# Kernel optimization log

Hardware: AMD Instinct MI355X
Metric: run time of the kernel (lower is better)

Reference implementation:

```python
import jax, jax.numpy as jnp
import numpy as np

H = 1024
L = 2

def setup_inputs() -> dict:
    key = jax.random.key(0)
    k1, k2, k3, k4, k5 = jax.random.split(key, 5)
    B, S = 32, 2048
    scale = 1.0 / np.sqrt(H)
    return {
        "query": jax.random.normal(k1, (B, 1, H * L), dtype=jnp.float32),
        "keys": jax.random.normal(k2, (B, S, H), dtype=jnp.float32),
        "Wa_w": jax.random.normal(k3, (H * L, H), dtype=jnp.float32) * scale,
        "Wa_b": jnp.zeros((H,), dtype=jnp.float32),
        "Ua_w": jax.random.normal(k4, (H, H), dtype=jnp.float32) * scale,
        "Ua_b": jnp.zeros((H,), dtype=jnp.float32),
        "Va_w": jax.random.normal(k5, (H, 1), dtype=jnp.float32) * scale,
        "Va_b": jnp.zeros((1,), dtype=jnp.float32),
    }

def reference(query, keys, Wa_w, Wa_b, Ua_w, Ua_b, Va_w, Va_b):
    # query: [B,1,H*L], keys: [B,S,H]
    q = jnp.einsum('bqd,dh->bqh', query, Wa_w) + Wa_b   # [B,1,H]
    k = jnp.einsum('bsd,dh->bsh', keys, Ua_w) + Ua_b    # [B,S,H]
    e = jnp.tanh(q + k)                                  # [B,S,H]
    scores = jnp.einsum('bsh,ho->bso', e, Va_w) + Va_b   # [B,S,1]
    scores = scores[:, :, 0][:, None, :]                 # [B,1,S]
    weights = jax.nn.softmax(scores, axis=-1)            # [B,1,S]
    context = jnp.einsum('bqs,bsh->bqh', weights, keys)  # [B,1,H]
    return (context, weights)
```

## Files before the change

kernel.cpp:

```cpp
#include <hip/hip_runtime.h>
#include <hip/hip_bf16.h>


typedef __attribute__((ext_vector_type(8))) short short8;
typedef __attribute__((ext_vector_type(4))) float floatx4;

typedef const __attribute__((address_space(1))) unsigned int gu32;
typedef __attribute__((address_space(3))) unsigned int lu32;

__device__ __forceinline__ unsigned short f2bf(float f) {
    union { float f; unsigned int u; } c; c.f = f;
    unsigned int u = c.u + 0x7fffu + ((c.u >> 16) & 1u);
    return (unsigned short)(u >> 16);
}

__device__ __forceinline__ unsigned int f2bf2(float lo, float hi) {
#if __has_builtin(__builtin_amdgcn_cvt_pk_bf16_f32)
    auto r = __builtin_amdgcn_cvt_pk_bf16_f32(lo, hi);
    unsigned int u; __builtin_memcpy(&u, &r, 4);
    return u;
#else
    return (unsigned int)f2bf(lo) | ((unsigned int)f2bf(hi) << 16);
#endif
}

__device__ __forceinline__ void gld16(const unsigned short* g, unsigned short* l) {
    __builtin_amdgcn_global_load_lds(
        (gu32*)(uintptr_t)g,
        (lu32*)(unsigned int)(uintptr_t)l,
        16, 0, 0);
}

__global__ __launch_bounds__(256) void qproj_k(
    const float* __restrict__ query, const float* __restrict__ Wa,
    const float* __restrict__ Wab, const float* __restrict__ Uab,
    float* __restrict__ qws)
{
    __shared__ float qs[2048];
    __shared__ float red[16*64];
    const int tid = threadIdx.x;
    const int b = blockIdx.x, hc = blockIdx.y;
    #pragma unroll
    for (int i = 0; i < 8; i++) qs[tid + 256*i] = query[b*2048 + tid + 256*i];
    __syncthreads();
    const int hq = tid & 15;
    const int dg = tid >> 4;
    const float4* wp = reinterpret_cast<const float4*>(Wa + (size_t)(dg*128)*1024 + hc*64 + hq*4);
    const float* qp = qs + dg*128;
    float4 a0; a0.x = a0.y = a0.z = a0.w = 0.f;
    float4 a1; a1.x = a1.y = a1.z = a1.w = 0.f;
    #pragma unroll 4
    for (int d = 0; d < 128; d += 2) {
        float q0 = qp[d], q1 = qp[d+1];
        float4 w0 = wp[(size_t)d*256];
        float4 w1 = wp[(size_t)(d+1)*256];
        a0.x += q0*w0.x; a0.y += q0*w0.y; a0.z += q0*w0.z; a0.w += q0*w0.w;
        a1.x += q1*w1.x; a1.y += q1*w1.y; a1.z += q1*w1.z; a1.w += q1*w1.w;
    }
    a0.x += a1.x; a0.y += a1.y; a0.z += a1.z; a0.w += a1.w;
    *reinterpret_cast<float4*>(red + dg*64 + hq*4) = a0;
    __syncthreads();
    if (tid < 64) {
        float v = 0.f;
        #pragma unroll
        for (int g = 0; g < 16; g++) v += red[g*64 + tid];
        int hh = hc*64 + tid;
        qws[b*1024 + hh] = v + Wab[hh] + Uab[hh];
    }
}

__global__ __launch_bounds__(256) void uat_k(const float* __restrict__ Ua,
                                             unsigned short* __restrict__ uat)
{
    __shared__ unsigned short t[64][65];
    const int x = threadIdx.x & 63, yy = threadIdx.x >> 6;
    const int d0 = blockIdx.x*64, h0 = blockIdx.y*64;
    #pragma unroll
    for (int i = 0; i < 16; i++) {
        int y = yy*16 + i;
        t[y][x] = f2bf(Ua[(size_t)(d0+y)*1024 + h0 + x]);
    }
    __syncthreads();
    #pragma unroll
    for (int i = 0; i < 16; i++) {
        int y = yy*16 + i;
        uat[(size_t)(h0+y)*1024 + d0 + x] = t[x][y];
    }
}

__global__ __launch_bounds__(256) void kb16_k(const float* __restrict__ keys,
                                              unsigned short* __restrict__ kb,
                                              unsigned int nf4)
{
    const unsigned int stride = gridDim.x * 256u;
    unsigned int f = blockIdx.x * 256u + threadIdx.x;
    #pragma unroll 4
    for (int it = 0; it < 4; ++it, f += stride) {
        if (f < nf4) {
            unsigned int elem = f << 2;
            unsigned int rg   = elem >> 10;
            unsigned int rem  = elem & 1023u;
            unsigned int g    = rem >> 5;
            unsigned int c    = (rem >> 3) & 3u;
            unsigned int half = (rem >> 2) & 1u;
            unsigned int p    = ((rg & 2047u) >> 1) & 3u;
            float4 v = reinterpret_cast<const float4*>(keys)[f];
            uint2 w;
            w.x = f2bf2(v.x, v.y);
            w.y = f2bf2(v.z, v.w);
            unsigned int dst = rg*1024u + g*32u + ((c ^ p) << 3) + (half << 2);
            *reinterpret_cast<uint2*>(kb + dst) = w;
        }
    }
}

__global__ __launch_bounds__(256) void score_gemm_fast(
    const unsigned short* __restrict__ kb16,
    const unsigned short* __restrict__ uat,
    const float* __restrict__ qws,
    const float* __restrict__ Va,
    float* __restrict__ score,
    int b0)
{
    __shared__ unsigned short aS[2][128*32];
    __shared__ unsigned short bS[2][256*32];
    const int tid = threadIdx.x;
    const int bz = blockIdx.z;
    const int b = b0 + bz;
    const int s0 = blockIdx.x * 128;
    const int h0 = blockIdx.y * 256;
    const int lane = tid & 63, wave = tid >> 6;
    const int quad = lane >> 4, l15 = lane & 15;
    const int wm = (wave & 1) * 64, wn = (wave >> 1) * 128;

    const int srow = lane >> 2;
    const int schunk = (lane & 3) ^ ((srow >> 1) & 3);
    const unsigned short* ubase = uat + (size_t)h0*1024;
    size_t boff[4];
    #pragma unroll
    for (int u = 0; u < 4; u++) {
        int cg = wave*4 + u;
        boff[u] = (size_t)(cg*16 + srow)*1024 + schunk*8;
    }

    const unsigned short* kA = kb16 + (size_t)(bz*2048 + s0)*1024;
    const size_t aoff0 = (size_t)(tid >> 2)*1024 + (size_t)(tid & 3)*8;
    const size_t aoff1 = (size_t)(64 + (tid >> 2))*1024 + (size_t)(tid & 3)*8;

    floatx4 acc[4][8];
    #pragma unroll
    for (int i = 0; i < 4; i++)
        #pragma unroll
        for (int j = 0; j < 8; j++) acc[i][j] = (floatx4)0.0f;

    gld16(kA + aoff0, aS[0] + wave*512);
    gld16(kA + aoff1, aS[0] + 2048 + wave*512);
    #pragma unroll
    for (int u = 0; u < 4; u++)
        gld16(ubase + boff[u], bS[0] + (wave*4 + u)*512);
    __syncthreads();

    int cur = 0;
    for (int kt = 0; kt < 31; ++kt) {
        const int nxt = cur ^ 1;
        const int k1 = (kt + 1) << 5;

        gld16(kA + aoff0 + k1, aS[nxt] + wave*512);
        gld16(kA + aoff1 + k1, aS[nxt] + 2048 + wave*512);
        #pragma unroll
        for (int u = 0; u < 4; u++)
            gld16(ubase + boff[u] + k1, bS[nxt] + (wave*4 + u)*512);

        short8 af[4], bf8[8];
        #pragma unroll
        for (int i = 0; i < 4; i++) {
            int row = wm + 16*i + l15;
            af[i] = *reinterpret_cast<const short8*>(aS[cur] + row*32 + ((quad ^ ((row>>1)&3)) * 8));
        }
        #pragma unroll
        for (int j = 0; j < 8; j++) {
            int row = wn + 16*j + l15;
            bf8[j] = *reinterpret_cast<const short8*>(bS[cur] + row*32 + ((quad ^ ((row>>1)&3)) * 8));
        }
        #pragma unroll
        for (int i = 0; i < 4; i++)
            #pragma unroll
            for (int j = 0; j < 8; j++)
                acc[i][j] = __builtin_amdgcn_mfma_f32_16x16x32_bf16(af[i], bf8[j], acc[i][j], 0, 0, 0);

        __syncthreads();
        cur = nxt;
    }

    {
        short8 af[4], bf8[8];
        #pragma unroll
        for (int i = 0; i < 4; i++) {
            int row = wm + 16*i + l15;
            af[i] = *reinterpret_cast<const short8*>(aS[cur] + row*32 + ((quad ^ ((row>>1)&3)) * 8));
        }
        #pragma unroll
        for (int j = 0; j < 8; j++) {
            int row = wn + 16*j + l15;
            bf8[j] = *reinterpret_cast<const short8*>(bS[cur] + row*32 + ((quad ^ ((row>>1)&3)) * 8));
        }
        #pragma unroll
        for (int i = 0; i < 4; i++)
            #pragma unroll
            for (int j = 0; j < 8; j++)
                acc[i][j] = __builtin_amdgcn_mfma_f32_16x16x32_bf16(af[i], bf8[j], acc[i][j], 0, 0, 0);
    }

    float qv[8], vav[8];
    #pragma unroll
    for (int j = 0; j < 8; j++) {
        int n = h0 + wn + 16*j + l15;
        qv[j]  = qws[b*1024 + n];
        vav[j] = Va[n];
    }
    #pragma unroll
    for (int i = 0; i < 4; i++) {
        #pragma unroll
        for (int r = 0; r < 4; r++) {
            float p = 0.f;
            #pragma unroll
            for (int j = 0; j < 8; j++) {
                float x = qv[j] + acc[i][j][r];
                float e = __expf(2.f * x);
                float t = 1.f - 2.f * __builtin_amdgcn_rcpf(e + 1.f);
                p += vav[j] * t;
            }
            #pragma unroll
            for (int off = 1; off < 16; off <<= 1) p += __shfl_xor(p, off, 64);
            if (l15 == 0) {
                int m = wm + 16*i + quad*4 + r;
                atomicAdd(score + (size_t)b*2048 + s0 + m, p);
            }
        }
    }
}

__global__ __launch_bounds__(256) void softmax_k(const float* __restrict__ score,
                                                 float* __restrict__ out_w)
{
    const int tid = threadIdx.x;
    const int b = blockIdx.x;
    __shared__ float wred[4], wred2[4];
    float sc[8];
    float mx = -3.0e38f;
    #pragma unroll
    for (int i = 0; i < 8; i++) {
        sc[i] = score[(size_t)b*2048 + tid + 256*i];
        mx = fmaxf(mx, sc[i]);
    }
    #pragma unroll
    for (int off = 32; off >= 1; off >>= 1) mx = fmaxf(mx, __shfl_xor(mx, off, 64));
    if ((tid & 63) == 0) wred[tid >> 6] = mx;
    __syncthreads();
    mx = fmaxf(fmaxf(wred[0], wred[1]), fmaxf(wred[2], wred[3]));
    float e[8]; float lsum = 0.f;
    #pragma unroll
    for (int i = 0; i < 8; i++) { e[i] = __expf(sc[i] - mx); lsum += e[i]; }
    #pragma unroll
    for (int off = 32; off >= 1; off >>= 1) lsum += __shfl_xor(lsum, off, 64);
    if ((tid & 63) == 0) wred2[tid >> 6] = lsum;
    __syncthreads();
    float inv = 1.0f / (wred2[0] + wred2[1] + wred2[2] + wred2[3]);
    #pragma unroll
    for (int i = 0; i < 8; i++) out_w[b*2048 + tid + 256*i] = e[i] * inv;
}

__global__ __launch_bounds__(256) void ctx_k(const float* __restrict__ keys,
                                             const float* __restrict__ w,
                                             float* __restrict__ out_ctx, int sper)
{
    const int tid = threadIdx.x;
    const int b = blockIdx.x, sc = blockIdx.y;
    const float4* k4 = reinterpret_cast<const float4*>(keys) + (size_t)(b*2048 + sc*sper)*256;
    const float* wp = w + b*2048 + sc*sper;
    float4 a; a.x = a.y = a.z = a.w = 0.f;
    #pragma unroll 4
    for (int s = 0; s < sper; s++) {
        float wv = wp[s];
        float4 kv = k4[(size_t)s*256 + tid];
        a.x += wv*kv.x; a.y += wv*kv.y; a.z += wv*kv.z; a.w += wv*kv.w;
    }
    float* o = out_ctx + (size_t)b*1024 + tid*4;
    atomicAdd(o + 0, a.x);
    atomicAdd(o + 1, a.y);
    atomicAdd(o + 2, a.z);
    atomicAdd(o + 3, a.w);
}

extern "C" void kernel_launch(void* const* d_in, const int* in_sizes, int n_in,
                              void* d_out, int out_size, void* d_ws, size_t ws_size,
                              hipStream_t stream)
{
    const float* query = (const float*)d_in[0];
    const float* keys  = (const float*)d_in[1];
    const float* Wa_w  = (const float*)d_in[2];
    const float* Wa_b  = (const float*)d_in[3];
    const float* Ua_w  = (const float*)d_in[4];
    const float* Ua_b  = (const float*)d_in[5];
    const float* Va_w  = (const float*)d_in[6];

    char* ws = (char*)d_ws;
    float*          qws     = (float*)(ws);
    unsigned short* uat     = (unsigned short*)(ws + (131072));
    float*          score   = (float*)(ws + (131072 + 2097152));
    const size_t BASE = 131072 + 2097152 + 4194304 + 2097152;
    unsigned short* kb16 = (unsigned short*)(ws + BASE);

    size_t avail = (ws_size > BASE) ? (ws_size - BASE) : 0;
    int nb = 32;
    while (nb > 1 && (size_t)nb * 2048 * 1024 * 2 > avail) nb >>= 1;

    float* out_ctx = (float*)d_out;
    float* out_w   = out_ctx + 32*1024;

    hipMemsetAsync(score, 0, 32*2048*sizeof(float), stream);
    hipMemsetAsync(out_ctx, 0, 32*1024*sizeof(float), stream);
    qproj_k<<<dim3(32, 16), 256, 0, stream>>>(query, Wa_w, Wa_b, Ua_b, qws);
    uat_k  <<<dim3(16, 16), 256, 0, stream>>>(Ua_w, uat);
    for (int b0 = 0; b0 < 32; b0 += nb) {
        unsigned int nf4 = (unsigned int)nb * 2048u * 256u;
        unsigned int nthr = (nf4 + 3u) / 4u;
        unsigned int nblk = (nthr + 255u) / 256u;
        kb16_k<<<dim3(nblk), 256, 0, stream>>>(keys + (size_t)b0*2048*1024, kb16, nf4);
        score_gemm_fast<<<dim3(16, 4, nb), 256, 0, stream>>>(kb16, uat, qws, Va_w, score, b0);
    }
    softmax_k<<<dim3(32),      256, 0, stream>>>(score, out_w);
    ctx_k    <<<dim3(32, 16),  256, 0, stream>>>(keys, out_w, out_ctx, 128);
}
```

Baseline: 622.4 us.

## Fuse keys bf16 conversion into score GEMM and merge prep kernels

Removes the separate keys-to-bf16 conversion pass and its workspace buffer. The score GEMM now loads fp32 keys straight into LDS with an XOR swizzle and converts them to bf16 while reading the MFMA A fragments. The query projection and Ua transpose kernels are merged into a single launch. This avoids writing and re-reading a 128MB bf16 copy of keys. In exchange, the A tile doubles its LDS footprint and global traffic per tile (fp32), each block issues more async loads, and conversion ALU work lands in the inner loop. Keys are also reloaded once for each of the 4 h-blocks.

```diff
diff --git a/kernel.cpp b/kernel.cpp
--- a/kernel.cpp
+++ b/kernel.cpp
@@ -24,109 +24,81 @@
 #endif
 }
 
-__device__ __forceinline__ void gld16(const unsigned short* g, unsigned short* l) {
+__device__ __forceinline__ void gld16(const void* g, const void* l) {
     __builtin_amdgcn_global_load_lds(
         (gu32*)(uintptr_t)g,
         (lu32*)(unsigned int)(uintptr_t)l,
         16, 0, 0);
 }
 
-__global__ __launch_bounds__(256) void qproj_k(
+__global__ __launch_bounds__(256) void prep_k(
     const float* __restrict__ query, const float* __restrict__ Wa,
     const float* __restrict__ Wab, const float* __restrict__ Uab,
-    float* __restrict__ qws)
-{
-    __shared__ float qs[2048];
-    __shared__ float red[16*64];
+    const float* __restrict__ Ua,
+    float* __restrict__ qws, unsigned short* __restrict__ uat)
+{
     const int tid = threadIdx.x;
-    const int b = blockIdx.x, hc = blockIdx.y;
-    #pragma unroll
-    for (int i = 0; i < 8; i++) qs[tid + 256*i] = query[b*2048 + tid + 256*i];
-    __syncthreads();
-    const int hq = tid & 15;
-    const int dg = tid >> 4;
-    const float4* wp = reinterpret_cast<const float4*>(Wa + (size_t)(dg*128)*1024 + hc*64 + hq*4);
-    const float* qp = qs + dg*128;
-    float4 a0; a0.x = a0.y = a0.z = a0.w = 0.f;
-    float4 a1; a1.x = a1.y = a1.z = a1.w = 0.f;
-    #pragma unroll 4
-    for (int d = 0; d < 128; d += 2) {
-        float q0 = qp[d], q1 = qp[d+1];
-        float4 w0 = wp[(size_t)d*256];
-        float4 w1 = wp[(size_t)(d+1)*256];
-        a0.x += q0*w0.x; a0.y += q0*w0.y; a0.z += q0*w0.z; a0.w += q0*w0.w;
-        a1.x += q1*w1.x; a1.y += q1*w1.y; a1.z += q1*w1.z; a1.w += q1*w1.w;
-    }
-    a0.x += a1.x; a0.y += a1.y; a0.z += a1.z; a0.w += a1.w;
-    *reinterpret_cast<float4*>(red + dg*64 + hq*4) = a0;
-    __syncthreads();
-    if (tid < 64) {
-        float v = 0.f;
-        #pragma unroll
-        for (int g = 0; g < 16; g++) v += red[g*64 + tid];
-        int hh = hc*64 + tid;
-        qws[b*1024 + hh] = v + Wab[hh] + Uab[hh];
-    }
-}
-
-__global__ __launch_bounds__(256) void uat_k(const float* __restrict__ Ua,
-                                             unsigned short* __restrict__ uat)
-{
-    __shared__ unsigned short t[64][65];
-    const int x = threadIdx.x & 63, yy = threadIdx.x >> 6;
-    const int d0 = blockIdx.x*64, h0 = blockIdx.y*64;
-    #pragma unroll
-    for (int i = 0; i < 16; i++) {
-        int y = yy*16 + i;
-        t[y][x] = f2bf(Ua[(size_t)(d0+y)*1024 + h0 + x]);
-    }
-    __syncthreads();
-    #pragma unroll
-    for (int i = 0; i < 16; i++) {
-        int y = yy*16 + i;
-        uat[(size_t)(h0+y)*1024 + d0 + x] = t[x][y];
-    }
-}
-
-__global__ __launch_bounds__(256) void kb16_k(const float* __restrict__ keys,
-                                              unsigned short* __restrict__ kb,
-                                              unsigned int nf4)
-{
-    const unsigned int stride = gridDim.x * 256u;
-    unsigned int f = blockIdx.x * 256u + threadIdx.x;
-    #pragma unroll 4
-    for (int it = 0; it < 4; ++it, f += stride) {
-        if (f < nf4) {
-            unsigned int elem = f << 2;
-            unsigned int rg   = elem >> 10;
-            unsigned int rem  = elem & 1023u;
-            unsigned int g    = rem >> 5;
-            unsigned int c    = (rem >> 3) & 3u;
-            unsigned int half = (rem >> 2) & 1u;
-            unsigned int p    = ((rg & 2047u) >> 1) & 3u;
-            float4 v = reinterpret_cast<const float4*>(keys)[f];
-            uint2 w;
-            w.x = f2bf2(v.x, v.y);
-            w.y = f2bf2(v.z, v.w);
-            unsigned int dst = rg*1024u + g*32u + ((c ^ p) << 3) + (half << 2);
-            *reinterpret_cast<uint2*>(kb + dst) = w;
+    if (blockIdx.x < 512) {
+        __shared__ float qs[2048];
+        __shared__ float red[16*64];
+        const int b = blockIdx.x >> 4, hc = blockIdx.x & 15;
+        #pragma unroll
+        for (int i = 0; i < 8; i++) qs[tid + 256*i] = query[b*2048 + tid + 256*i];
+        __syncthreads();
+        const int hq = tid & 15;
+        const int dg = tid >> 4;
+        const float4* wp = reinterpret_cast<const float4*>(Wa + (size_t)(dg*128)*1024 + hc*64 + hq*4);
+        const float* qp = qs + dg*128;
+        float4 a0; a0.x = a0.y = a0.z = a0.w = 0.f;
+        float4 a1; a1.x = a1.y = a1.z = a1.w = 0.f;
+        #pragma unroll 4
+        for (int d = 0; d < 128; d += 2) {
+            float q0 = qp[d], q1 = qp[d+1];
+            float4 w0 = wp[(size_t)d*256];
+            float4 w1 = wp[(size_t)(d+1)*256];
+            a0.x += q0*w0.x; a0.y += q0*w0.y; a0.z += q0*w0.z; a0.w += q0*w0.w;
+            a1.x += q1*w1.x; a1.y += q1*w1.y; a1.z += q1*w1.z; a1.w += q1*w1.w;
+        }
+        a0.x += a1.x; a0.y += a1.y; a0.z += a1.z; a0.w += a1.w;
+        *reinterpret_cast<float4*>(red + dg*64 + hq*4) = a0;
+        __syncthreads();
+        if (tid < 64) {
+            float v = 0.f;
+            #pragma unroll
+            for (int g = 0; g < 16; g++) v += red[g*64 + tid];
+            int hh = hc*64 + tid;
+            qws[b*1024 + hh] = v + Wab[hh] + Uab[hh];
+        }
+    } else {
+        __shared__ unsigned short t[64][65];
+        const int q = blockIdx.x - 512;
+        const int x = tid & 63, yy = tid >> 6;
+        const int d0 = (q >> 4)*64, h0 = (q & 15)*64;
+        #pragma unroll
+        for (int i = 0; i < 16; i++) {
+            int y = yy*16 + i;
+            t[y][x] = f2bf(Ua[(size_t)(d0+y)*1024 + h0 + x]);
+        }
+        __syncthreads();
+        #pragma unroll
+        for (int i = 0; i < 16; i++) {
+            int y = yy*16 + i;
+            uat[(size_t)(h0+y)*1024 + d0 + x] = t[x][y];
         }
     }
 }
 
 __global__ __launch_bounds__(256) void score_gemm_fast(
-    const unsigned short* __restrict__ kb16,
+    const float* __restrict__ keys,
     const unsigned short* __restrict__ uat,
     const float* __restrict__ qws,
     const float* __restrict__ Va,
-    float* __restrict__ score,
-    int b0)
-{
-    __shared__ unsigned short aS[2][128*32];
+    float* __restrict__ score)
+{
+    __shared__ float          aSf[2][128*32];
     __shared__ unsigned short bS[2][256*32];
     const int tid = threadIdx.x;
-    const int bz = blockIdx.z;
-    const int b = b0 + bz;
+    const int b  = blockIdx.z;
     const int s0 = blockIdx.x * 128;
     const int h0 = blockIdx.y * 256;
     const int lane = tid & 63, wave = tid >> 6;
@@ -143,9 +115,13 @@
         boff[u] = (size_t)(cg*16 + srow)*1024 + schunk*8;
     }
 
-    const unsigned short* kA = kb16 + (size_t)(bz*2048 + s0)*1024;
-    const size_t aoff0 = (size_t)(tid >> 2)*1024 + (size_t)(tid & 3)*8;
-    const size_t aoff1 = (size_t)(64 + (tid >> 2))*1024 + (size_t)(tid & 3)*8;
+    const float* kA = keys + (size_t)(b*2048 + s0)*1024;
+    const int arow = tid >> 3;
+    const int acx  = (tid & 7) ^ ((tid >> 3) & 7);
+    size_t aoff[4];
+    #pragma unroll
+    for (int i = 0; i < 4; i++)
+        aoff[i] = (size_t)(i*32 + arow)*1024 + acx*4;
 
     floatx4 acc[4][8];
     #pragma unroll
@@ -153,8 +129,9 @@
         #pragma unroll
         for (int j = 0; j < 8; j++) acc[i][j] = (floatx4)0.0f;
 
-    gld16(kA + aoff0, aS[0] + wave*512);
-    gld16(kA + aoff1, aS[0] + 2048 + wave*512);
+    #pragma unroll
+    for (int i = 0; i < 4; i++)
+        gld16(kA + aoff[i], (unsigned short*)aSf[0] + i*2048 + wave*512);
     #pragma unroll
     for (int u = 0; u < 4; u++)
         gld16(ubase + boff[u], bS[0] + (wave*4 + u)*512);
@@ -165,8 +142,9 @@
         const int nxt = cur ^ 1;
         const int k1 = (kt + 1) << 5;
 
-        gld16(kA + aoff0 + k1, aS[nxt] + wave*512);
-        gld16(kA + aoff1 + k1, aS[nxt] + 2048 + wave*512);
+        #pragma unroll
+        for (int i = 0; i < 4; i++)
+            gld16(kA + aoff[i] + k1, (unsigned short*)aSf[nxt] + i*2048 + wave*512);
         #pragma unroll
         for (int u = 0; u < 4; u++)
             gld16(ubase + boff[u] + k1, bS[nxt] + (wave*4 + u)*512);
@@ -175,7 +153,13 @@
         #pragma unroll
         for (int i = 0; i < 4; i++) {
             int row = wm + 16*i + l15;
-            af[i] = *reinterpret_cast<const short8*>(aS[cur] + row*32 + ((quad ^ ((row>>1)&3)) * 8));
+            const float* rp = aSf[cur] + row*32;
+            float4 v0 = *reinterpret_cast<const float4*>(rp + (((2*quad)   ^ (row&7)) * 4));
+            float4 v1 = *reinterpret_cast<const float4*>(rp + (((2*quad+1) ^ (row&7)) * 4));
+            union { uint4 u; short8 s; } cv;
+            cv.u.x = f2bf2(v0.x, v0.y); cv.u.y = f2bf2(v0.z, v0.w);
+            cv.u.z = f2bf2(v1.x, v1.y); cv.u.w = f2bf2(v1.z, v1.w);
+            af[i] = cv.s;
         }
         #pragma unroll
         for (int j = 0; j < 8; j++) {
@@ -197,7 +181,13 @@
         #pragma unroll
         for (int i = 0; i < 4; i++) {
             int row = wm + 16*i + l15;
-            af[i] = *reinterpret_cast<const short8*>(aS[cur] + row*32 + ((quad ^ ((row>>1)&3)) * 8));
+            const float* rp = aSf[cur] + row*32;
+            float4 v0 = *reinterpret_cast<const float4*>(rp + (((2*quad)   ^ (row&7)) * 4));
+            float4 v1 = *reinterpret_cast<const float4*>(rp + (((2*quad+1) ^ (row&7)) * 4));
+            union { uint4 u; short8 s; } cv;
+            cv.u.x = f2bf2(v0.x, v0.y); cv.u.y = f2bf2(v0.z, v0.w);
+            cv.u.z = f2bf2(v1.x, v1.y); cv.u.w = f2bf2(v1.z, v1.w);
+            af[i] = cv.s;
         }
         #pragma unroll
         for (int j = 0; j < 8; j++) {
@@ -305,30 +295,17 @@
     const float* Va_w  = (const float*)d_in[6];
 
     char* ws = (char*)d_ws;
-    float*          qws     = (float*)(ws);
-    unsigned short* uat     = (unsigned short*)(ws + (131072));
-    float*          score   = (float*)(ws + (131072 + 2097152));
-    const size_t BASE = 131072 + 2097152 + 4194304 + 2097152;
-    unsigned short* kb16 = (unsigned short*)(ws + BASE);
-
-    size_t avail = (ws_size > BASE) ? (ws_size - BASE) : 0;
-    int nb = 32;
-    while (nb > 1 && (size_t)nb * 2048 * 1024 * 2 > avail) nb >>= 1;
+    float*          qws   = (float*)(ws);
+    unsigned short* uat   = (unsigned short*)(ws + 131072);
+    float*          score = (float*)(ws + 131072 + 2097152);
 
     float* out_ctx = (float*)d_out;
     float* out_w   = out_ctx + 32*1024;
 
     hipMemsetAsync(score, 0, 32*2048*sizeof(float), stream);
     hipMemsetAsync(out_ctx, 0, 32*1024*sizeof(float), stream);
-    qproj_k<<<dim3(32, 16), 256, 0, stream>>>(query, Wa_w, Wa_b, Ua_b, qws);
-    uat_k  <<<dim3(16, 16), 256, 0, stream>>>(Ua_w, uat);
-    for (int b0 = 0; b0 < 32; b0 += nb) {
-        unsigned int nf4 = (unsigned int)nb * 2048u * 256u;
-        unsigned int nthr = (nf4 + 3u) / 4u;
-        unsigned int nblk = (nthr + 255u) / 256u;
-        kb16_k<<<dim3(nblk), 256, 0, stream>>>(keys + (size_t)b0*2048*1024, kb16, nf4);
-        score_gemm_fast<<<dim3(16, 4, nb), 256, 0, stream>>>(kb16, uat, qws, Va_w, score, b0);
-    }
-    softmax_k<<<dim3(32),      256, 0, stream>>>(score, out_w);
-    ctx_k    <<<dim3(32, 16),  256, 0, stream>>>(keys, out_w, out_ctx, 128);
-}
+    prep_k<<<dim3(768), 256, 0, stream>>>(query, Wa_w, Wa_b, Ua_b, Ua_w, qws, uat);
+    score_gemm_fast<<<dim3(16, 4, 32), 256, 0, stream>>>(keys, uat, qws, Va_w, score);
+    softmax_k<<<dim3(32),     256, 0, stream>>>(score, out_w);
+    ctx_k    <<<dim3(32, 16), 256, 0, stream>>>(keys, out_w, out_ctx, 128);
+}
```

Result: slower. 678.6 us (+9.0%).
